# Kernel optimization log

Measured on AMD Instinct MI355X. Metric: run time of the kernel, lower is better.

Reference implementation:

```python
import jax, jax.numpy as jnp
import numpy as np

T, N, F_IN = 5, 10000, 16
E = 160000
C = 32          # gat_hidden_dim (per head)
H0 = 2          # heads in layer 0 (concat) -> out 64
GRU = 64
OUT_H = 32


def setup_inputs() -> dict:
    key = jax.random.key(0)
    ks = jax.random.split(key, 24)
    s = 0.1
    inp = {
        "x_seq": jax.random.normal(ks[0], (T, N, F_IN), jnp.float32),
        "edge_index": jax.random.randint(ks[1], (2, E), 0, N, jnp.int32),
        # GAT layer 0: in 16 -> 2 heads x 32, concat -> 64
        "gat0_W": s * jax.random.normal(ks[2], (F_IN, H0 * C), jnp.float32),
        "gat0_asrc": s * jax.random.normal(ks[3], (H0, C), jnp.float32),
        "gat0_adst": s * jax.random.normal(ks[4], (H0, C), jnp.float32),
        "gat0_b": s * jax.random.normal(ks[5], (H0 * C,), jnp.float32),
        "res0_W": s * jax.random.normal(ks[6], (F_IN, H0 * C), jnp.float32),   # [in,out]
        # GAT layer 1: in 64 -> 1 head x 32, no concat -> 32
        "gat1_W": s * jax.random.normal(ks[7], (H0 * C, C), jnp.float32),
        "gat1_asrc": s * jax.random.normal(ks[8], (1, C), jnp.float32),
        "gat1_adst": s * jax.random.normal(ks[9], (1, C), jnp.float32),
        "gat1_b": s * jax.random.normal(ks[10], (C,), jnp.float32),
        "res1_W": s * jax.random.normal(ks[11], (H0 * C, C), jnp.float32),
        # GRU cells (torch GRUCell layout: W_i [3H,in], W_h [3H,H])
        "gru0_Wi": s * jax.random.normal(ks[12], (3 * GRU, C), jnp.float32),
        "gru0_Wh": s * jax.random.normal(ks[13], (3 * GRU, GRU), jnp.float32),
        "gru0_bi": s * jax.random.normal(ks[14], (3 * GRU,), jnp.float32),
        "gru0_bh": s * jax.random.normal(ks[15], (3 * GRU,), jnp.float32),
        "gru1_Wi": s * jax.random.normal(ks[16], (3 * GRU, GRU), jnp.float32),
        "gru1_Wh": s * jax.random.normal(ks[17], (3 * GRU, GRU), jnp.float32),
        "gru1_bi": s * jax.random.normal(ks[18], (3 * GRU,), jnp.float32),
        "gru1_bh": s * jax.random.normal(ks[19], (3 * GRU,), jnp.float32),
        # MLP head
        "fc1_W": s * jax.random.normal(ks[20], (GRU, OUT_H), jnp.float32),
        "fc1_b": s * jax.random.normal(ks[21], (OUT_H,), jnp.float32),
        "fc2_W": s * jax.random.normal(ks[22], (OUT_H, 1), jnp.float32),
        "fc2_b": s * jax.random.normal(ks[23], (1,), jnp.float32),
    }
    return inp


def _gat(x, src, dst, n, W, a_src, a_dst, b, heads, concat):
    ch = W.shape[1] // heads
    xw = (x @ W).reshape(n, heads, ch)                      # [N,H,C]
    al_s = (xw * a_src).sum(-1)                             # [N,H]
    al_d = (xw * a_dst).sum(-1)
    e = jax.nn.leaky_relu(al_s[src] + al_d[dst], 0.2)       # [Etot,H]
    m = jax.ops.segment_max(e, dst, num_segments=n)
    ex = jnp.exp(e - m[dst])
    den = jax.ops.segment_sum(ex, dst, num_segments=n)
    alpha = ex / (den[dst] + 1e-16)                         # scatter-softmax
    out = jax.ops.segment_sum(alpha[:, :, None] * xw[src], dst, num_segments=n)
    out = out.reshape(n, heads * ch) if concat else out.mean(axis=1)
    return out + b


def _gru(x, h, Wi, Wh, bi, bh):
    gi = x @ Wi.T + bi
    gh = h @ Wh.T + bh
    i_r, i_z, i_n = jnp.split(gi, 3, axis=-1)
    h_r, h_z, h_n = jnp.split(gh, 3, axis=-1)
    r = jax.nn.sigmoid(i_r + h_r)
    z = jax.nn.sigmoid(i_z + h_z)
    nn_ = jnp.tanh(i_n + r * h_n)
    return (1.0 - z) * nn_ + z * h


def reference(x_seq, edge_index,
              gat0_W, gat0_asrc, gat0_adst, gat0_b, res0_W,
              gat1_W, gat1_asrc, gat1_adst, gat1_b, res1_W,
              gru0_Wi, gru0_Wh, gru0_bi, gru0_bh,
              gru1_Wi, gru1_Wh, gru1_bi, gru1_bh,
              fc1_W, fc1_b, fc2_W, fc2_b):
    n = x_seq.shape[1]
    loops = jnp.arange(n, dtype=edge_index.dtype)
    src = jnp.concatenate([edge_index[0], loops])           # PyG adds self-loops
    dst = jnp.concatenate([edge_index[1], loops])

    def step(carry, x_t):
        h0, h1 = carry
        x1 = jax.nn.elu(_gat(x_t, src, dst, n, gat0_W, gat0_asrc, gat0_adst, gat0_b, 2, True)) + x_t @ res0_W
        x2 = jax.nn.elu(_gat(x1, src, dst, n, gat1_W, gat1_asrc, gat1_adst, gat1_b, 1, False)) + x1 @ res1_W
        h0 = _gru(x2, h0, gru0_Wi, gru0_Wh, gru0_bi, gru0_bh)
        h1 = _gru(h0, h1, gru1_Wi, gru1_Wh, gru1_bi, gru1_bh)
        return (h0, h1), None

    h0 = jnp.zeros((n, gru0_Wh.shape[1]), x_seq.dtype)
    h1 = jnp.zeros((n, gru1_Wh.shape[1]), x_seq.dtype)
    (h0, h1), _ = jax.lax.scan(step, (h0, h1), x_seq)
    h = jax.nn.relu(h1 @ fc1_W + fc1_b)
    return h @ fc2_W + fc2_b                                # [N,1]
```

## Files before the change

kernel.cpp:

```cpp
#include <hip/hip_runtime.h>
#include <hip/hip_bf16.h>
#include <math.h>

#define T_STEPS 5
#define NNODES  10000
#define NM      (T_STEPS * NNODES)
#define F_IN    16
#define NEDGES  160000
#define ETOT    (NEDGES + NNODES)
#define GW      8
#define GNPW    5

#define CNT_BLKS 665
#define TRN_BLKS 216
#define MM0_BLKS 12500

#define RL(v, k)  __int_as_float(__builtin_amdgcn_readlane(__float_as_int(v), (k)))
#define RLI(v, k) __builtin_amdgcn_readlane((v), (k))

__global__ __launch_bounds__(1024) void k_scan(const int* __restrict__ counts, int* __restrict__ offs) {
    __shared__ int sc[NNODES];
    __shared__ int ssum[1024];
    int t = threadIdx.x;
    for (int i = t; i < NNODES; i += 1024) sc[i] = counts[i];
    __syncthreads();
    const int chunk = (NNODES + 1023) / 1024;
    int start = t * chunk, end = min(start + chunk, NNODES);
    int s = 0;
    for (int i = start; i < end; i++) s += sc[i];
    ssum[t] = s;
    __syncthreads();
    for (int off = 1; off < 1024; off <<= 1) {
        int v = (t >= off) ? ssum[t - off] : 0;
        __syncthreads();
        ssum[t] += v;
        __syncthreads();
    }
    int excl = (t == 0) ? 0 : ssum[t - 1];
    for (int i = start; i < end; i++) { int c = sc[i]; sc[i] = excl; excl += c; }
    __syncthreads();
    for (int i = t; i < NNODES; i += 1024) offs[i] = sc[i];
    if (t == 1023) offs[NNODES] = ssum[1023];
}

__global__ __launch_bounds__(256) void k_fill(const int* __restrict__ ei, const int* __restrict__ offs,
                                              int* __restrict__ cursor, int* __restrict__ csr) {
    int idx = blockIdx.x * 256 + threadIdx.x;
    if (idx >= ETOT) return;
    int src, dst;
    if (idx < NEDGES) { src = ei[idx]; dst = ei[NEDGES + idx]; }
    else              { src = dst = idx - NEDGES; }
    int p = atomicAdd(&cursor[dst], 1);
    csr[offs[dst] + p] = src;
}

__global__ __launch_bounds__(256) void k_preamble(const int* __restrict__ ei, int* __restrict__ counts,
                                                  const float* __restrict__ Wi0, const float* __restrict__ Wh0,
                                                  const float* __restrict__ Wi1, const float* __restrict__ Wh1,
                                                  float* __restrict__ WiT0, float* __restrict__ WhT0,
                                                  float* __restrict__ WiT1, float* __restrict__ WhT1,
                                                  float2* __restrict__ h0rz, float* __restrict__ h0n,
                                                  float2* __restrict__ i1rz, float* __restrict__ i1n,
                                                  float2* __restrict__ h1rz, float* __restrict__ h1n,
                                                  const float* __restrict__ x,
                                                  const float* __restrict__ W,
                                                  const float* __restrict__ Wres,
                                                  const float* __restrict__ asrc, const float* __restrict__ adst,
                                                  float* __restrict__ xw, float* __restrict__ xres,
                                                  float* __restrict__ als, float* __restrict__ ald) {
    int b = blockIdx.x;
    if (b < CNT_BLKS) {
        int idx = b * 256 + threadIdx.x;
        if (idx >= ETOT) return;
        int dst = (idx < NEDGES) ? ei[NEDGES + idx] : (idx - NEDGES);
        atomicAdd(&counts[dst], 1);
        return;
    }
    if (b < CNT_BLKS + TRN_BLKS) {
        int idx = (b - CNT_BLKS) * 256 + threadIdx.x;
        if (idx < 6144)  { int k = idx / 192, r = idx % 192; WiT0[idx] = Wi0[r * 32 + k]; return; }
        idx -= 6144;
        if (idx < 12288) { int k = idx / 192, r = idx % 192; WhT0[idx] = Wh0[r * 64 + k]; return; }
        idx -= 12288;
        if (idx < 12288) { int k = idx / 192, r = idx % 192; WiT1[idx] = Wi1[r * 64 + k]; return; }
        idx -= 12288;
        if (idx < 12288) { int k = idx / 192, r = idx % 192; WhT1[idx] = Wh1[r * 64 + k]; return; }
        idx -= 12288;
        if (idx < 4096) { int k = idx >> 6, c = idx & 63;
                          h0rz[idx] = make_float2(Wh0[c * 64 + k], Wh0[(64 + c) * 64 + k]);
                          h0n[idx]  = Wh0[(128 + c) * 64 + k]; return; }
        idx -= 4096;
        if (idx < 4096) { int k = idx >> 6, c = idx & 63;
                          i1rz[idx] = make_float2(Wi1[c * 64 + k], Wi1[(64 + c) * 64 + k]);
                          i1n[idx]  = Wi1[(128 + c) * 64 + k]; return; }
        idx -= 4096;
        if (idx < 4096) { int k = idx >> 6, c = idx & 63;
                          h1rz[idx] = make_float2(Wh1[c * 64 + k], Wh1[(64 + c) * 64 + k]);
                          h1n[idx]  = Wh1[(128 + c) * 64 + k]; }
        return;
    }
    int wave = threadIdx.x >> 6, lane = threadIdx.x & 63;
    int m = (b - CNT_BLKS - TRN_BLKS) * 4 + wave;
    if (m >= NM) return;
    const float* xr = x + (size_t)m * F_IN;
    float xreg[F_IN];
#pragma unroll
    for (int k = 0; k < F_IN; k++) xreg[k] = xr[k];
    float acc = 0.f, accr = 0.f;
#pragma unroll
    for (int k = 0; k < F_IN; k++) {
        acc  += xreg[k] * W[k * 64 + lane];
        accr += xreg[k] * Wres[k * 64 + lane];
    }
    xw[(size_t)m * 64 + lane]   = acc;
    xres[(size_t)m * 64 + lane] = accr;
    float ps = acc * asrc[lane], pd = acc * adst[lane];
    for (int off = 16; off; off >>= 1) {
        ps += __shfl_down(ps, off, 32);
        pd += __shfl_down(pd, off, 32);
    }
    if ((lane & 31) == 0) {
        int h = lane >> 5;
        als[m * 2 + h] = ps;
        ald[m * 2 + h] = pd;
    }
}

__global__ __launch_bounds__(256) void k_gat0_all(const float* __restrict__ xw,
                                                  const float* __restrict__ xres,
                                                  const float* __restrict__ als,
                                                  const float* __restrict__ ald,
                                                  const int* __restrict__ offs, const int* __restrict__ csr,
                                                  const float* __restrict__ b,
                                                  const float* __restrict__ W1,
                                                  const float* __restrict__ Wres1,
                                                  const float* __restrict__ as1,
                                                  const float* __restrict__ ad1v,
                                                  float* __restrict__ xw1, float* __restrict__ xres1,
                                                  float* __restrict__ als1, float* __restrict__ ald1) {
    int wave = threadIdx.x >> 6, lane = threadIdx.x & 63;
    int m = blockIdx.x * 4 + wave;
    if (m >= NM) return;
    int t = m / NNODES;
    int node = m - t * NNODES;
    int base = t * NNODES;
    int beg = offs[node], end = offs[node + 1];
    int deg = end - beg;
    float xresv = xres[(size_t)m * 64 + lane];
    float ad0 = ald[m * 2 + 0], ad1 = ald[m * 2 + 1];
    float acc;
    if (deg <= 64) {
        int s = 0; float e0 = -INFINITY, e1 = -INFINITY;
        if (lane < deg) {
            s = base + csr[beg + lane];
            e0 = als[s * 2 + 0] + ad0; e0 = e0 > 0.f ? e0 : 0.2f * e0;
            e1 = als[s * 2 + 1] + ad1; e1 = e1 > 0.f ? e1 : 0.2f * e1;
        }
        float m0 = e0, m1 = e1;
        for (int o = 32; o; o >>= 1) {
            m0 = fmaxf(m0, __shfl_xor(m0, o));
            m1 = fmaxf(m1, __shfl_xor(m1, o));
        }
        float ex0 = (lane < deg) ? __expf(e0 - m0) : 0.f;
        float ex1 = (lane < deg) ? __expf(e1 - m1) : 0.f;
        float d0 = ex0, d1 = ex1;
        for (int o = 32; o; o >>= 1) {
            d0 += __shfl_xor(d0, o);
            d1 += __shfl_xor(d1, o);
        }
        ex0 *= 1.f / (d0 + 1e-16f);
        ex1 *= 1.f / (d1 + 1e-16f);
        float a0 = 0.f, a1 = 0.f, a2 = 0.f, a3 = 0.f;
        int i = 0;
        for (; i + 8 <= deg; i += 8) {
            int   s0 = RLI(s, i),    s1 = RLI(s, i+1), s2 = RLI(s, i+2), s3 = RLI(s, i+3);
            int   s4 = RLI(s, i+4),  s5 = RLI(s, i+5), s6 = RLI(s, i+6), s7 = RLI(s, i+7);
            float x0 = xw[(size_t)s0 * 64 + lane];
            float x1 = xw[(size_t)s1 * 64 + lane];
            float x2 = xw[(size_t)s2 * 64 + lane];
            float x3 = xw[(size_t)s3 * 64 + lane];
            float x4 = xw[(size_t)s4 * 64 + lane];
            float x5 = xw[(size_t)s5 * 64 + lane];
            float x6 = xw[(size_t)s6 * 64 + lane];
            float x7 = xw[(size_t)s7 * 64 + lane];
            float u0 = (lane < 32) ? RL(ex0, i)   : RL(ex1, i);
            float u1 = (lane < 32) ? RL(ex0, i+1) : RL(ex1, i+1);
            float u2 = (lane < 32) ? RL(ex0, i+2) : RL(ex1, i+2);
            float u3 = (lane < 32) ? RL(ex0, i+3) : RL(ex1, i+3);
            float u4 = (lane < 32) ? RL(ex0, i+4) : RL(ex1, i+4);
            float u5 = (lane < 32) ? RL(ex0, i+5) : RL(ex1, i+5);
            float u6 = (lane < 32) ? RL(ex0, i+6) : RL(ex1, i+6);
            float u7 = (lane < 32) ? RL(ex0, i+7) : RL(ex1, i+7);
            a0 += u0 * x0 + u4 * x4;
            a1 += u1 * x1 + u5 * x5;
            a2 += u2 * x2 + u6 * x6;
            a3 += u3 * x3 + u7 * x7;
        }
        for (; i < deg; i++) {
            int s0 = RLI(s, i);
            float u = (lane < 32) ? RL(ex0, i) : RL(ex1, i);
            a0 += u * xw[(size_t)s0 * 64 + lane];
        }
        acc = (a0 + a1) + (a2 + a3);
    } else {
        float m0 = -INFINITY, m1 = -INFINITY;
        for (int i = beg + lane; i < end; i += 64) {
            int s = base + csr[i];
            float e0 = als[s * 2 + 0] + ad0; e0 = e0 > 0.f ? e0 : 0.2f * e0;
            float e1 = als[s * 2 + 1] + ad1; e1 = e1 > 0.f ? e1 : 0.2f * e1;
            m0 = fmaxf(m0, e0); m1 = fmaxf(m1, e1);
        }
        for (int o = 32; o; o >>= 1) {
            m0 = fmaxf(m0, __shfl_xor(m0, o));
            m1 = fmaxf(m1, __shfl_xor(m1, o));
        }
        float d0 = 0.f, d1 = 0.f;
        for (int i = beg + lane; i < end; i += 64) {
            int s = base + csr[i];
            float e0 = als[s * 2 + 0] + ad0; e0 = e0 > 0.f ? e0 : 0.2f * e0;
            float e1 = als[s * 2 + 1] + ad1; e1 = e1 > 0.f ? e1 : 0.2f * e1;
            d0 += __expf(e0 - m0); d1 += __expf(e1 - m1);
        }
        for (int o = 32; o; o >>= 1) { d0 += __shfl_xor(d0, o); d1 += __shfl_xor(d1, o); }
        float inv0 = 1.f / (d0 + 1e-16f), inv1 = 1.f / (d1 + 1e-16f);
        acc = 0.f;
        for (int i = beg; i < end; i++) {
            int s = base + csr[i];
            float e, wgt;
            if (lane < 32) { e = als[s * 2 + 0] + ad0; e = e > 0.f ? e : 0.2f * e; wgt = __expf(e - m0) * inv0; }
            else           { e = als[s * 2 + 1] + ad1; e = e > 0.f ? e : 0.2f * e; wgt = __expf(e - m1) * inv1; }
            acc += wgt * xw[(size_t)s * 64 + lane];
        }
    }
    float x1v = acc + b[lane];
    x1v = x1v > 0.f ? x1v : expm1f(x1v);
    x1v += xresv;
    int j = lane & 31;
    const float* Wp = (lane < 32) ? W1 : Wres1;
    float pacc = 0.f;
#pragma unroll
    for (int k = 0; k < 64; k++) {
        float xv = RL(x1v, k);
        pacc += xv * Wp[k * 32 + j];
    }
    if (lane < 32) xw1[(size_t)m * 32 + j]   = pacc;
    else           xres1[(size_t)m * 32 + j] = pacc;
    float ps = (lane < 32) ? pacc * as1[j]  : 0.f;
    float pd = (lane < 32) ? pacc * ad1v[j] : 0.f;
    for (int o = 16; o; o >>= 1) {
        ps += __shfl_down(ps, o, 32);
        pd += __shfl_down(pd, o, 32);
    }
    if (lane == 0) { als1[m] = ps; ald1[m] = pd; }
}

__global__ __launch_bounds__(256) void k_gat1_all(const float* __restrict__ xw1,
                                                  const float* __restrict__ xres1,
                                                  const float* __restrict__ als1,
                                                  const float* __restrict__ ald1,
                                                  const int* __restrict__ offs, const int* __restrict__ csr,
                                                  const float* __restrict__ b,
                                                  const float* __restrict__ WiT0,
                                                  const float* __restrict__ bi0,
                                                  float* __restrict__ gi0) {
    int wave = threadIdx.x >> 6, lane = threadIdx.x & 63;
    int m = blockIdx.x * 4 + wave;
    if (m >= NM) return;
    int t = m / NNODES;
    int node = m - t * NNODES;
    int base = t * NNODES;
    int beg = offs[node], end = offs[node + 1];
    int deg = end - beg;
    int ch = lane & 31, half = lane >> 5;
    float xres1v = xres1[(size_t)m * 32 + ch];
    float adv = ald1[m];
    float aggr;
    if (deg <= 64) {
        int s = 0; float e = -INFINITY;
        if (lane < deg) {
            s = base + csr[beg + lane];
            e = als1[s] + adv; e = e > 0.f ? e : 0.2f * e;
        }
        float mx = e;
        for (int o = 32; o; o >>= 1) mx = fmaxf(mx, __shfl_xor(mx, o));
        float ex = (lane < deg) ? __expf(e - mx) : 0.f;
        float d = ex;
        for (int o = 32; o; o >>= 1) d += __shfl_xor(d, o);
        ex *= 1.f / (d + 1e-16f);
        float acc0 = 0.f, acc1 = 0.f;
        int i = 0;
        for (; i + 8 <= deg; i += 8) {
            int   e0 = RLI(s, i),   o0 = RLI(s, i+1);
            int   e1 = RLI(s, i+2), o1 = RLI(s, i+3);
            int   e2 = RLI(s, i+4), o2 = RLI(s, i+5);
            int   e3 = RLI(s, i+6), o3 = RLI(s, i+7);
            int   sa0 = half ? o0 : e0, sa1 = half ? o1 : e1;
            int   sa2 = half ? o2 : e2, sa3 = half ? o3 : e3;
            float xa0 = xw1[(size_t)sa0 * 32 + ch];
            float xa1 = xw1[(size_t)sa1 * 32 + ch];
            float xa2 = xw1[(size_t)sa2 * 32 + ch];
            float xa3 = xw1[(size_t)sa3 * 32 + ch];
            float we0 = RL(ex, i),   wo0 = RL(ex, i+1);
            float we1 = RL(ex, i+2), wo1 = RL(ex, i+3);
            float we2 = RL(ex, i+4), wo2 = RL(ex, i+5);
            float we3 = RL(ex, i+6), wo3 = RL(ex, i+7);
            float wa0 = half ? wo0 : we0, wa1 = half ? wo1 : we1;
            float wa2 = half ? wo2 : we2, wa3 = half ? wo3 : we3;
            acc0 += wa0 * xa0 + wa2 * xa2;
            acc1 += wa1 * xa1 + wa3 * xa3;
        }
        for (; i < deg; i += 2) {
            int i2 = (i + 1 < deg) ? i + 1 : i;
            int   sa = RLI(s, i),  sb = RLI(s, i2);
            float wa = RL(ex, i),  wb = RL(ex, i2);
            if (i + 1 >= deg) wb = 0.f;
            int   sm = half ? sb : sa;
            float wm = half ? wb : wa;
            acc0 += wm * xw1[(size_t)sm * 32 + ch];
        }
        float acc = acc0 + acc1;
        acc += __shfl_xor(acc, 32);
        aggr = acc;
    } else {
        float mx = -INFINITY;
        for (int i = beg + lane; i < end; i += 64) {
            float e = als1[base + csr[i]] + adv; e = e > 0.f ? e : 0.2f * e;
            mx = fmaxf(mx, e);
        }
        for (int o = 32; o; o >>= 1) mx = fmaxf(mx, __shfl_xor(mx, o));
        float d = 0.f;
        for (int i = beg + lane; i < end; i += 64) {
            float e = als1[base + csr[i]] + adv; e = e > 0.f ? e : 0.2f * e;
            d += __expf(e - mx);
        }
        for (int o = 32; o; o >>= 1) d += __shfl_xor(d, o);
        float inv = 1.f / (d + 1e-16f);
        float acc = 0.f;
        for (int i = beg; i < end; i++) {
            int s = base + csr[i];
            float e = als1[s] + adv; e = e > 0.f ? e : 0.2f * e;
            float wgt = __expf(e - mx) * inv;
            acc += wgt * xw1[(size_t)s * 32 + ch];
        }
        aggr = acc;
    }
    float v = aggr + b[ch];
    v = v > 0.f ? v : expm1f(v);
    float x2v = v + xres1v;
    float p0 = bi0[lane], p1 = bi0[64 + lane], p2 = bi0[128 + lane];
#pragma unroll 8
    for (int k = 0; k < 32; k++) {
        float xv = RL(x2v, k);
        p0 += xv * WiT0[k * 192 + lane];
        p1 += xv * WiT0[k * 192 + 64 + lane];
        p2 += xv * WiT0[k * 192 + 128 + lane];
    }
    gi0[(size_t)m * 192 + lane]       = p0;
    gi0[(size_t)m * 192 + 64 + lane]  = p1;
    gi0[(size_t)m * 192 + 128 + lane] = p2;
}

__global__ __launch_bounds__(512) void k_gruhead_p(const float* __restrict__ gi0,
                                                   const float4* __restrict__ wblob,
                                                   const float* __restrict__ bh0,
                                                   const float* __restrict__ bi1, const float* __restrict__ bh1,
                                                   const float* __restrict__ fc1W, const float* __restrict__ fc1b,
                                                   const float* __restrict__ fc2W, const float* __restrict__ fc2b,
                                                   float* __restrict__ out) {
    extern __shared__ char ldsraw[];
    float2* Lh0rz = (float2*)ldsraw;
    float*  Lh0n  = (float*)(ldsraw + 32768);
    float2* Li1rz = (float2*)(ldsraw + 49152);
    float*  Li1n  = (float*)(ldsraw + 81920);
    float2* Lh1rz = (float2*)(ldsraw + 98304);
    float*  Lh1n  = (float*)(ldsraw + 131072);
    int tid = threadIdx.x, wave = tid >> 6, lane = tid & 63;
    int node0 = (blockIdx.x * GW + wave) * GNPW;

    {
        float4* D = (float4*)ldsraw;
#pragma unroll
        for (int i = 0; i < 18; i++) D[tid + i * 512] = wblob[tid + i * 512];
    }

    float pr[GNPW], pz[GNPW], pn[GNPW];
#pragma unroll
    for (int n = 0; n < GNPW; n++) {
        size_t gb = ((size_t)node0 + n) * 192;
        pr[n] = gi0[gb + lane];
        pz[n] = gi0[gb + 64 + lane];
        pn[n] = gi0[gb + 128 + lane];
    }
    __syncthreads();

    float bhr0 = bh0[lane], bhz0 = bh0[64 + lane], bhn0 = bh0[128 + lane];
    float bir1 = bi1[lane] + bh1[lane];
    float biz1 = bi1[64 + lane] + bh1[64 + lane];
    float bin1 = bi1[128 + lane], bhn1 = bh1[128 + lane];

    float h0[GNPW] = {0.f, 0.f, 0.f, 0.f, 0.f};
    float h1[GNPW] = {0.f, 0.f, 0.f, 0.f, 0.f};

    for (int t = 0; t < T_STEPS; t++) {
        float gr[GNPW], gz[GNPW], gin[GNPW], ghn[GNPW];
#pragma unroll
        for (int n = 0; n < GNPW; n++) {
            gr[n]  = pr[n] + bhr0;
            gz[n]  = pz[n] + bhz0;
            gin[n] = pn[n];
            ghn[n] = bhn0;
        }
        if (t + 1 < T_STEPS) {
            size_t gb1 = ((size_t)(t + 1) * NNODES + node0) * 192;
#pragma unroll
            for (int n = 0; n < GNPW; n++) {
                pr[n] = gi0[gb1 + n * 192 + lane];
                pz[n] = gi0[gb1 + n * 192 + 64 + lane];
                pn[n] = gi0[gb1 + n * 192 + 128 + lane];
            }
        }
#pragma unroll 8
        for (int k = 0; k < 64; k++) {
            float2 wrz = Lh0rz[k * 64 + lane];
            float  wn  = Lh0n[k * 64 + lane];
#pragma unroll
            for (int n = 0; n < GNPW; n++) {
                float hv = RL(h0[n], k);
                gr[n] += hv * wrz.x; gz[n] += hv * wrz.y; ghn[n] += hv * wn;
            }
        }
#pragma unroll
        for (int n = 0; n < GNPW; n++) {
            float r = 1.f / (1.f + __expf(-gr[n]));
            float z = 1.f / (1.f + __expf(-gz[n]));
            float nn = tanhf(gin[n] + r * ghn[n]);
            h0[n] = (1.f - z) * nn + z * h0[n];
        }

#pragma unroll
        for (int n = 0; n < GNPW; n++) { gr[n] = bir1; gz[n] = biz1; gin[n] = bin1; }
#pragma unroll 8
        for (int k = 0; k < 64; k++) {
            float2 wrz = Li1rz[k * 64 + lane];
            float  wn  = Li1n[k * 64 + lane];
#pragma unroll
            for (int n = 0; n < GNPW; n++) {
                float xv = RL(h0[n], k);
                gr[n] += xv * wrz.x; gz[n] += xv * wrz.y; gin[n] += xv * wn;
            }
        }
#pragma unroll
        for (int n = 0; n < GNPW; n++) ghn[n] = bhn1;
#pragma unroll 8
        for (int k = 0; k < 64; k++) {
            float2 wrz = Lh1rz[k * 64 + lane];
            float  wn  = Lh1n[k * 64 + lane];
#pragma unroll
            for (int n = 0; n < GNPW; n++) {
                float hv = RL(h1[n], k);
                gr[n] += hv * wrz.x; gz[n] += hv * wrz.y; ghn[n] += hv * wn;
            }
        }
#pragma unroll
        for (int n = 0; n < GNPW; n++) {
            float r = 1.f / (1.f + __expf(-gr[n]));
            float z = 1.f / (1.f + __expf(-gz[n]));
            float nn = tanhf(gin[n] + r * ghn[n]);
            h1[n] = (1.f - z) * nn + z * h1[n];
        }
    }

    int j = lane & 31, half = lane >> 5;
#pragma unroll
    for (int p = 0; p < 3; p++) {
        int ne = 2 * p;
        int no = (2 * p + 1 < GNPW) ? 2 * p + 1 : 2 * p;
        float a = fc1b[j];
#pragma unroll
        for (int k = 0; k < 64; k++) {
            float he = RL(h1[ne], k);
            float ho = RL(h1[no], k);
            a += (half ? ho : he) * fc1W[k * 32 + j];
        }
        a = fmaxf(a, 0.f);
        float v = a * fc2W[j];
        for (int o = 16; o; o >>= 1) v += __shfl_down(v, o, 32);
        if ((lane & 31) == 0 && 2 * p + half < GNPW) out[node0 + 2 * p + half] = v + fc2b[0];
    }
}

__global__ __launch_bounds__(512) void k_gruhead(const float* __restrict__ gi0,
                                                 const float* __restrict__ WhT0,
                                                 const float* __restrict__ WiT1,
                                                 const float* __restrict__ WhT1,
                                                 const float* __restrict__ bh0,
                                                 const float* __restrict__ bi1, const float* __restrict__ bh1,
                                                 const float* __restrict__ fc1W, const float* __restrict__ fc1b,
                                                 const float* __restrict__ fc2W, const float* __restrict__ fc2b,
                                                 float* __restrict__ out) {
    __shared__ float lw[64 * 192];
    int tid = threadIdx.x;
    int wave = tid >> 6, lane = tid & 63;
    int node0 = (blockIdx.x * GW + wave) * GNPW;

    float bhr0 = bh0[lane], bhz0 = bh0[64 + lane], bhn0 = bh0[128 + lane];
    float bir1 = bi1[lane] + bh1[lane];
    float biz1 = bi1[64 + lane] + bh1[64 + lane];
    float bin1 = bi1[128 + lane], bhn1 = bh1[128 + lane];

    float h0[GNPW] = {0.f, 0.f, 0.f, 0.f, 0.f};
    float h1[GNPW] = {0.f, 0.f, 0.f, 0.f, 0.f};

    auto stage = [&](const float* __restrict__ src) {
        __syncthreads();
        const float4* s4 = (const float4*)src;
        float4* d4 = (float4*)lw;
#pragma unroll
        for (int i = 0; i < 6; i++) d4[tid + i * 512] = s4[tid + i * 512];
        __syncthreads();
    };

    for (int t = 0; t < T_STEPS; t++) {
        float gr[GNPW], gz[GNPW], gin[GNPW], ghn[GNPW];
        size_t gb = ((size_t)t * NNODES + node0) * 192;
#pragma unroll
        for (int n = 0; n < GNPW; n++) {
            gr[n]  = gi0[gb + n * 192 + lane] + bhr0;
            gz[n]  = gi0[gb + n * 192 + 64 + lane] + bhz0;
            gin[n] = gi0[gb + n * 192 + 128 + lane];
            ghn[n] = bhn0;
        }
        stage(WhT0);
#pragma unroll 4
        for (int k = 0; k < 64; k++) {
            float wr = lw[k * 192 + lane];
            float wz = lw[k * 192 + 64 + lane];
            float wn = lw[k * 192 + 128 + lane];
#pragma unroll
            for (int n = 0; n < GNPW; n++) {
                float hv = RL(h0[n], k);
                gr[n] += hv * wr; gz[n] += hv * wz; ghn[n] += hv * wn;
            }
        }
#pragma unroll
        for (int n = 0; n < GNPW; n++) {
            float r = 1.f / (1.f + __expf(-gr[n]));
            float z = 1.f / (1.f + __expf(-gz[n]));
            float nn = tanhf(gin[n] + r * ghn[n]);
            h0[n] = (1.f - z) * nn + z * h0[n];
        }
#pragma unroll
        for (int n = 0; n < GNPW; n++) { gr[n] = bir1; gz[n] = biz1; gin[n] = bin1; }
        stage(WiT1);
#pragma unroll 4
        for (int k = 0; k < 64; k++) {
            float wir = lw[k * 192 + lane];
            float wiz = lw[k * 192 + 64 + lane];
            float win = lw[k * 192 + 128 + lane];
#pragma unroll
            for (int n = 0; n < GNPW; n++) {
                float xv = RL(h0[n], k);
                gr[n] += xv * wir; gz[n] += xv * wiz; gin[n] += xv * win;
            }
        }
#pragma unroll
        for (int n = 0; n < GNPW; n++) ghn[n] = bhn1;
        stage(WhT1);
#pragma unroll 4
        for (int k = 0; k < 64; k++) {
            float whr = lw[k * 192 + lane];
            float whz = lw[k * 192 + 64 + lane];
            float whn = lw[k * 192 + 128 + lane];
#pragma unroll
            for (int n = 0; n < GNPW; n++) {
                float hv = RL(h1[n], k);
                gr[n] += hv * whr; gz[n] += hv * whz; ghn[n] += hv * whn;
            }
        }
#pragma unroll
        for (int n = 0; n < GNPW; n++) {
            float r = 1.f / (1.f + __expf(-gr[n]));
            float z = 1.f / (1.f + __expf(-gz[n]));
            float nn = tanhf(gin[n] + r * ghn[n]);
            h1[n] = (1.f - z) * nn + z * h1[n];
        }
    }

    int j = lane & 31, half = lane >> 5;
#pragma unroll
    for (int p = 0; p < 3; p++) {
        int ne = 2 * p;
        int no = (2 * p + 1 < GNPW) ? 2 * p + 1 : 2 * p;
        float a = fc1b[j];
#pragma unroll
        for (int k = 0; k < 64; k++) {
            float he = RL(h1[ne], k);
            float ho = RL(h1[no], k);
            a += (half ? ho : he) * fc1W[k * 32 + j];
        }
        a = fmaxf(a, 0.f);
        float v = a * fc2W[j];
        for (int o = 16; o; o >>= 1) v += __shfl_down(v, o, 32);
        if ((lane & 31) == 0 && 2 * p + half < GNPW) out[node0 + 2 * p + half] = v + fc2b[0];
    }
}

extern "C" void kernel_launch(void* const* d_in, const int* in_sizes, int n_in,
                              void* d_out, int out_size, void* d_ws, size_t ws_size,
                              hipStream_t stream) {
    const float* x_seq   = (const float*)d_in[0];
    const int*   ei      = (const int*)d_in[1];
    const float* gat0_W  = (const float*)d_in[2];
    const float* gat0_as = (const float*)d_in[3];
    const float* gat0_ad = (const float*)d_in[4];
    const float* gat0_b  = (const float*)d_in[5];
    const float* res0_W  = (const float*)d_in[6];
    const float* gat1_W  = (const float*)d_in[7];
    const float* gat1_as = (const float*)d_in[8];
    const float* gat1_ad = (const float*)d_in[9];
    const float* gat1_b  = (const float*)d_in[10];
    const float* res1_W  = (const float*)d_in[11];
    const float* gru0_Wi = (const float*)d_in[12];
    const float* gru0_Wh = (const float*)d_in[13];
    const float* gru0_bi = (const float*)d_in[14];
    const float* gru0_bh = (const float*)d_in[15];
    const float* gru1_Wi = (const float*)d_in[16];
    const float* gru1_Wh = (const float*)d_in[17];
    const float* gru1_bi = (const float*)d_in[18];
    const float* gru1_bh = (const float*)d_in[19];
    const float* fc1_W   = (const float*)d_in[20];
    const float* fc1_b   = (const float*)d_in[21];
    const float* fc2_W   = (const float*)d_in[22];
    const float* fc2_b   = (const float*)d_in[23];
    float* out = (float*)d_out;

    char* w = (char*)d_ws;
    size_t off = 0;
    auto take = [&](size_t bytes) { size_t r = off; off += (bytes + 255) & ~(size_t)255; return r; };
    const size_t N = NNODES, M = NM;
    int*   counts = (int*)(w + take(N * 4));
    int*   cursor = (int*)(w + take(N * 4));
    size_t zero_span = off;
    int*   offs   = (int*)(w + take((N + 1) * 4));
    int*   csr    = (int*)(w + take((size_t)ETOT * 4));
    float* xw0    = (float*)(w + take(M * 64 * 4));
    float* xres0  = (float*)(w + take(M * 64 * 4));
    float* als0   = (float*)(w + take(M * 2 * 4));
    float* ald0   = (float*)(w + take(M * 2 * 4));
    float* xw1    = (float*)(w + take(M * 32 * 4));
    float* xres1  = (float*)(w + take(M * 32 * 4));
    float* als1   = (float*)(w + take(M * 4));
    float* ald1   = (float*)(w + take(M * 4));
    float* gi0    = (float*)(w + take(M * 192 * 4));
    float* wiT0   = (float*)(w + take(32 * 192 * 4));
    float* whT0   = (float*)(w + take(64 * 192 * 4));
    float* wiT1   = (float*)(w + take(64 * 192 * 4));
    float* whT1   = (float*)(w + take(64 * 192 * 4));
    char*   blob  = w + take(147456);
    float2* h0rz  = (float2*)blob;
    float*  h0n   = (float*)(blob + 32768);
    float2* i1rz  = (float2*)(blob + 49152);
    float*  i1n   = (float*)(blob + 81920);
    float2* h1rz  = (float2*)(blob + 98304);
    float*  h1n   = (float*)(blob + 131072);

    hipMemsetAsync(w, 0, zero_span, stream);

    k_preamble<<<CNT_BLKS + TRN_BLKS + MM0_BLKS, 256, 0, stream>>>(
        ei, counts,
        gru0_Wi, gru0_Wh, gru1_Wi, gru1_Wh,
        wiT0, whT0, wiT1, whT1,
        h0rz, h0n, i1rz, i1n, h1rz, h1n,
        x_seq, gat0_W, res0_W, gat0_as, gat0_ad, xw0, xres0, als0, ald0);

    k_scan<<<1, 1024, 0, stream>>>(counts, offs);
    k_fill<<<CNT_BLKS, 256, 0, stream>>>(ei, offs, cursor, csr);

    k_gat0_all<<<MM0_BLKS, 256, 0, stream>>>(xw0, xres0, als0, ald0, offs, csr, gat0_b,
                                             gat1_W, res1_W, gat1_as, gat1_ad,
                                             xw1, xres1, als1, ald1);
    k_gat1_all<<<MM0_BLKS, 256, 0, stream>>>(xw1, xres1, als1, ald1, offs, csr, gat1_b,
                                             wiT0, gru0_bi, gi0);

    const int ggrid = NNODES / (GW * GNPW);
    hipError_t ae = hipFuncSetAttribute(reinterpret_cast<const void*>(k_gruhead_p),
                                        hipFuncAttributeMaxDynamicSharedMemorySize, 147456);
    if (ae == hipSuccess) {
        k_gruhead_p<<<ggrid, 512, 147456, stream>>>(gi0, (const float4*)blob,
                                                    gru0_bh, gru1_bi, gru1_bh,
                                                    fc1_W, fc1_b, fc2_W, fc2_b, out);
    } else {
        k_gruhead<<<ggrid, 512, 0, stream>>>(gi0, whT0, wiT1, whT1,
                                             gru0_bh, gru1_bi, gru1_bh,
                                             fc1_W, fc1_b, fc2_W, fc2_b, out);
    }
}
```

Before: 357.6 us.

## Rebalance GRU head to 1024-thread blocks with split LDS/global weights

```diff
diff --git a/kernel.cpp b/kernel.cpp
--- a/kernel.cpp
+++ b/kernel.cpp
@@ -360,51 +360,37 @@
     gi0[(size_t)m * 192 + 128 + lane] = p2;
 }
 
-__global__ __launch_bounds__(512) void k_gruhead_p(const float* __restrict__ gi0,
-                                                   const float4* __restrict__ wblob,
-                                                   const float* __restrict__ bh0,
-                                                   const float* __restrict__ bi1, const float* __restrict__ bh1,
-                                                   const float* __restrict__ fc1W, const float* __restrict__ fc1b,
-                                                   const float* __restrict__ fc2W, const float* __restrict__ fc2b,
-                                                   float* __restrict__ out) {
-    extern __shared__ char ldsraw[];
-    float2* Lh0rz = (float2*)ldsraw;
-    float*  Lh0n  = (float*)(ldsraw + 32768);
-    float2* Li1rz = (float2*)(ldsraw + 49152);
-    float*  Li1n  = (float*)(ldsraw + 81920);
-    float2* Lh1rz = (float2*)(ldsraw + 98304);
-    float*  Lh1n  = (float*)(ldsraw + 131072);
-    int tid = threadIdx.x, wave = tid >> 6, lane = tid & 63;
-    int node0 = (blockIdx.x * GW + wave) * GNPW;
-
-    {
-        float4* D = (float4*)ldsraw;
-#pragma unroll
-        for (int i = 0; i < 18; i++) D[tid + i * 512] = wblob[tid + i * 512];
-    }
-
-    float pr[GNPW], pz[GNPW], pn[GNPW];
-#pragma unroll
-    for (int n = 0; n < GNPW; n++) {
+template <int NPW>
+__device__ __forceinline__ void gru_chain(int node0, int lane,
+                                          const float* __restrict__ gi0,
+                                          const float2* Lh0rz, const float2* Li1rz, const float2* Lh1rz,
+                                          const float* __restrict__ h0nG, const float* __restrict__ i1nG,
+                                          const float* __restrict__ h1nG,
+                                          const float* __restrict__ bh0,
+                                          const float* __restrict__ bi1, const float* __restrict__ bh1,
+                                          const float* __restrict__ fc1W, const float* __restrict__ fc1b,
+                                          const float* __restrict__ fc2W, const float* __restrict__ fc2b,
+                                          float* __restrict__ out) {
+    float bhr0 = bh0[lane], bhz0 = bh0[64 + lane], bhn0 = bh0[128 + lane];
+    float bir1 = bi1[lane] + bh1[lane];
+    float biz1 = bi1[64 + lane] + bh1[64 + lane];
+    float bin1 = bi1[128 + lane], bhn1 = bh1[128 + lane];
+
+    float h0[NPW], h1[NPW], pr[NPW], pz[NPW], pn[NPW];
+#pragma unroll
+    for (int n = 0; n < NPW; n++) { h0[n] = 0.f; h1[n] = 0.f; }
+#pragma unroll
+    for (int n = 0; n < NPW; n++) {
         size_t gb = ((size_t)node0 + n) * 192;
         pr[n] = gi0[gb + lane];
         pz[n] = gi0[gb + 64 + lane];
         pn[n] = gi0[gb + 128 + lane];
     }
-    __syncthreads();
-
-    float bhr0 = bh0[lane], bhz0 = bh0[64 + lane], bhn0 = bh0[128 + lane];
-    float bir1 = bi1[lane] + bh1[lane];
-    float biz1 = bi1[64 + lane] + bh1[64 + lane];
-    float bin1 = bi1[128 + lane], bhn1 = bh1[128 + lane];
-
-    float h0[GNPW] = {0.f, 0.f, 0.f, 0.f, 0.f};
-    float h1[GNPW] = {0.f, 0.f, 0.f, 0.f, 0.f};
 
     for (int t = 0; t < T_STEPS; t++) {
-        float gr[GNPW], gz[GNPW], gin[GNPW], ghn[GNPW];
-#pragma unroll
-        for (int n = 0; n < GNPW; n++) {
+        float gr[NPW], gz[NPW], gin[NPW], ghn[NPW];
+#pragma unroll
+        for (int n = 0; n < NPW; n++) {
             gr[n]  = pr[n] + bhr0;
             gz[n]  = pz[n] + bhz0;
             gin[n] = pn[n];
@@ -413,7 +399,7 @@
         if (t + 1 < T_STEPS) {
             size_t gb1 = ((size_t)(t + 1) * NNODES + node0) * 192;
 #pragma unroll
-            for (int n = 0; n < GNPW; n++) {
+            for (int n = 0; n < NPW; n++) {
                 pr[n] = gi0[gb1 + n * 192 + lane];
                 pz[n] = gi0[gb1 + n * 192 + 64 + lane];
                 pn[n] = gi0[gb1 + n * 192 + 128 + lane];
@@ -422,47 +408,40 @@
 #pragma unroll 8
         for (int k = 0; k < 64; k++) {
             float2 wrz = Lh0rz[k * 64 + lane];
-            float  wn  = Lh0n[k * 64 + lane];
-#pragma unroll
-            for (int n = 0; n < GNPW; n++) {
+            float  wn  = h0nG[k * 64 + lane];
+#pragma unroll
+            for (int n = 0; n < NPW; n++) {
                 float hv = RL(h0[n], k);
                 gr[n] += hv * wrz.x; gz[n] += hv * wrz.y; ghn[n] += hv * wn;
             }
         }
 #pragma unroll
-        for (int n = 0; n < GNPW; n++) {
+        for (int n = 0; n < NPW; n++) {
             float r = 1.f / (1.f + __expf(-gr[n]));
             float z = 1.f / (1.f + __expf(-gz[n]));
             float nn = tanhf(gin[n] + r * ghn[n]);
             h0[n] = (1.f - z) * nn + z * h0[n];
         }
-
-#pragma unroll
-        for (int n = 0; n < GNPW; n++) { gr[n] = bir1; gz[n] = biz1; gin[n] = bin1; }
+#pragma unroll
+        for (int n = 0; n < NPW; n++) { gr[n] = bir1; gz[n] = biz1; gin[n] = bin1; ghn[n] = bhn1; }
 #pragma unroll 8
         for (int k = 0; k < 64; k++) {
-            float2 wrz = Li1rz[k * 64 + lane];
-            float  wn  = Li1n[k * 64 + lane];
-#pragma unroll
-            for (int n = 0; n < GNPW; n++) {
+            float2 wirz = Li1rz[k * 64 + lane];
+            float  win  = i1nG[k * 64 + lane];
+            float2 whrz = Lh1rz[k * 64 + lane];
+            float  whn  = h1nG[k * 64 + lane];
+#pragma unroll
+            for (int n = 0; n < NPW; n++) {
                 float xv = RL(h0[n], k);
-                gr[n] += xv * wrz.x; gz[n] += xv * wrz.y; gin[n] += xv * wn;
+                float hv = RL(h1[n], k);
+                gr[n]  += xv * wirz.x + hv * whrz.x;
+                gz[n]  += xv * wirz.y + hv * whrz.y;
+                gin[n] += xv * win;
+                ghn[n] += hv * whn;
             }
         }
 #pragma unroll
-        for (int n = 0; n < GNPW; n++) ghn[n] = bhn1;
-#pragma unroll 8
-        for (int k = 0; k < 64; k++) {
-            float2 wrz = Lh1rz[k * 64 + lane];
-            float  wn  = Lh1n[k * 64 + lane];
-#pragma unroll
-            for (int n = 0; n < GNPW; n++) {
-                float hv = RL(h1[n], k);
-                gr[n] += hv * wrz.x; gz[n] += hv * wrz.y; ghn[n] += hv * wn;
-            }
-        }
-#pragma unroll
-        for (int n = 0; n < GNPW; n++) {
+        for (int n = 0; n < NPW; n++) {
             float r = 1.f / (1.f + __expf(-gr[n]));
             float z = 1.f / (1.f + __expf(-gz[n]));
             float nn = tanhf(gin[n] + r * ghn[n]);
@@ -472,9 +451,9 @@
 
     int j = lane & 31, half = lane >> 5;
 #pragma unroll
-    for (int p = 0; p < 3; p++) {
+    for (int p = 0; p < (NPW + 1) / 2; p++) {
         int ne = 2 * p;
-        int no = (2 * p + 1 < GNPW) ? 2 * p + 1 : 2 * p;
+        int no = (2 * p + 1 < NPW) ? 2 * p + 1 : 2 * p;
         float a = fc1b[j];
 #pragma unroll
         for (int k = 0; k < 64; k++) {
@@ -485,7 +464,39 @@
         a = fmaxf(a, 0.f);
         float v = a * fc2W[j];
         for (int o = 16; o; o >>= 1) v += __shfl_down(v, o, 32);
-        if ((lane & 31) == 0 && 2 * p + half < GNPW) out[node0 + 2 * p + half] = v + fc2b[0];
+        if ((lane & 31) == 0 && 2 * p + half < NPW) out[node0 + 2 * p + half] = v + fc2b[0];
+    }
+}
+
+__global__ __launch_bounds__(1024) void k_gruhead_p(const float* __restrict__ gi0,
+                                                    const float4* __restrict__ rzblob,
+                                                    const float* __restrict__ h0nG,
+                                                    const float* __restrict__ i1nG,
+                                                    const float* __restrict__ h1nG,
+                                                    const float* __restrict__ bh0,
+                                                    const float* __restrict__ bi1, const float* __restrict__ bh1,
+                                                    const float* __restrict__ fc1W, const float* __restrict__ fc1b,
+                                                    const float* __restrict__ fc2W, const float* __restrict__ fc2b,
+                                                    float* __restrict__ out) {
+    extern __shared__ char ldsraw[];
+    float2* Lh0rz = (float2*)ldsraw;
+    float2* Li1rz = (float2*)(ldsraw + 32768);
+    float2* Lh1rz = (float2*)(ldsraw + 65536);
+    int tid = threadIdx.x, wave = tid >> 6, lane = tid & 63;
+    {
+        float4* D = (float4*)ldsraw;
+#pragma unroll
+        for (int i = 0; i < 6; i++) D[tid + i * 1024] = rzblob[tid + i * 1024];
+    }
+    __syncthreads();
+
+    int bb = blockIdx.x * 40;
+    if (wave < 8) {
+        gru_chain<3>(bb + wave * 3, lane, gi0, Lh0rz, Li1rz, Lh1rz, h0nG, i1nG, h1nG,
+                     bh0, bi1, bh1, fc1W, fc1b, fc2W, fc2b, out);
+    } else {
+        gru_chain<2>(bb + 24 + (wave - 8) * 2, lane, gi0, Lh0rz, Li1rz, Lh1rz, h0nG, i1nG, h1nG,
+                     bh0, bi1, bh1, fc1W, fc1b, fc2W, fc2b, out);
     }
 }
 
@@ -656,13 +667,13 @@
     float* whT0   = (float*)(w + take(64 * 192 * 4));
     float* wiT1   = (float*)(w + take(64 * 192 * 4));
     float* whT1   = (float*)(w + take(64 * 192 * 4));
-    char*   blob  = w + take(147456);
-    float2* h0rz  = (float2*)blob;
-    float*  h0n   = (float*)(blob + 32768);
-    float2* i1rz  = (float2*)(blob + 49152);
-    float*  i1n   = (float*)(blob + 81920);
-    float2* h1rz  = (float2*)(blob + 98304);
-    float*  h1n   = (float*)(blob + 131072);
+    char*   rzb   = w + take(98304);
+    float2* h0rz  = (float2*)rzb;
+    float2* i1rz  = (float2*)(rzb + 32768);
+    float2* h1rz  = (float2*)(rzb + 65536);
+    float*  h0n   = (float*)(w + take(4096 * 4));
+    float*  i1n   = (float*)(w + take(4096 * 4));
+    float*  h1n   = (float*)(w + take(4096 * 4));
 
     hipMemsetAsync(w, 0, zero_span, stream);
 
@@ -682,16 +693,15 @@
     k_gat1_all<<<MM0_BLKS, 256, 0, stream>>>(xw1, xres1, als1, ald1, offs, csr, gat1_b,
                                              wiT0, gru0_bi, gi0);
 
-    const int ggrid = NNODES / (GW * GNPW);
     hipError_t ae = hipFuncSetAttribute(reinterpret_cast<const void*>(k_gruhead_p),
-                                        hipFuncAttributeMaxDynamicSharedMemorySize, 147456);
+                                        hipFuncAttributeMaxDynamicSharedMemorySize, 98304);
     if (ae == hipSuccess) {
-        k_gruhead_p<<<ggrid, 512, 147456, stream>>>(gi0, (const float4*)blob,
-                                                    gru0_bh, gru1_bi, gru1_bh,
-                                                    fc1_W, fc1_b, fc2_W, fc2_b, out);
+        k_gruhead_p<<<250, 1024, 98304, stream>>>(gi0, (const float4*)rzb, h0n, i1n, h1n,
+                                                  gru0_bh, gru1_bi, gru1_bh,
+                                                  fc1_W, fc1_b, fc2_W, fc2_b, out);
     } else {
-        k_gruhead<<<ggrid, 512, 0, stream>>>(gi0, whT0, wiT1, whT1,
-                                             gru0_bh, gru1_bi, gru1_bh,
-                                             fc1_W, fc1_b, fc2_W, fc2_b, out);
-    }
-}
+        k_gruhead<<<NNODES / (GW * GNPW), 512, 0, stream>>>(gi0, whT0, wiT1, whT1,
+                                                            gru0_bh, gru1_bi, gru1_bh,
+                                                            fc1_W, fc1_b, fc2_W, fc2_b, out);
+    }
+}
```

After: 375.9 us. 5.1% more time.
